# Performance work log

Measured on AMD Instinct MI355X. Metric: run time of the kernel, lower is better.

## Reference

```python
import jax, jax.numpy as jnp
import numpy as np

N = 50000   # nodes
E = 800000  # edges (avg degree 16)
D = 128     # in_dim == hidden_dim


def setup_inputs() -> dict:
    key = jax.random.key(0)
    ks = jax.random.split(key, 8)
    x = jax.random.normal(ks[0], (N, D), dtype=jnp.float32)
    edge_index = jax.random.randint(ks[1], (2, E), 0, N, dtype=jnp.int32)
    s = 1.0 / np.sqrt(D)  # glorot-ish scale
    W0 = jax.random.normal(ks[2], (D, D), dtype=jnp.float32) * s
    W1 = jax.random.normal(ks[3], (D, D), dtype=jnp.float32) * s
    W2 = jax.random.normal(ks[4], (D, D), dtype=jnp.float32) * s
    b0 = jnp.zeros((D,), dtype=jnp.float32)
    b1 = jnp.zeros((D,), dtype=jnp.float32)
    b2 = jnp.zeros((D,), dtype=jnp.float32)
    return {"x": x, "edge_index": edge_index,
            "W0": W0, "b0": b0, "W1": W1, "b1": b1, "W2": W2, "b2": b2}


def reference(x, edge_index, W0, b0, W1, b1, W2, b2):
    # PyG GCNConv defaults: add self-loops, symmetric D^-1/2 (A+I) D^-1/2 norm,
    # linear transform first, bias added after aggregation.
    src, dst = edge_index[0], edge_index[1]
    loops = jnp.arange(N, dtype=src.dtype)
    src_f = jnp.concatenate([src, loops])  # [E+N]
    dst_f = jnp.concatenate([dst, loops])
    deg = jax.ops.segment_sum(jnp.ones_like(src_f, dtype=x.dtype), dst_f, num_segments=N)
    dinv = jnp.where(deg > 0, jax.lax.rsqrt(deg), 0.0)
    norm = dinv[src_f] * dinv[dst_f]  # [E+N]

    def gcn_layer(h, W, b):
        h = h @ W                                # [N, D]
        msg = h[src_f] * norm[:, None]           # [E+N, D] gather
        agg = jax.ops.segment_sum(msg, dst_f, num_segments=N)  # scatter-add
        return agg + b

    h = jax.nn.relu(gcn_layer(x, W0, b0))  # dropout p=0.0 is a no-op
    h = jax.nn.relu(gcn_layer(h, W1, b1))
    return gcn_layer(h, W2, b2)
```

## Files before the change

kernel.cpp:

```cpp
#include <hip/hip_runtime.h>
#include <hip/hip_fp16.h>

#define NN 50000
#define NPAD 50048
#define NE 800000
#define D 128
#define BPAD 136
#define EGRID 3125
#define NB 196
#define GGRID 782

typedef __attribute__((ext_vector_type(8))) short bf16x8;
typedef __attribute__((ext_vector_type(4))) float f32x4;

__device__ inline unsigned short f2bf(float f) {
    unsigned int b = __float_as_uint(f);
    return (unsigned short)((b + 0x7FFFu + ((b >> 16) & 1u)) >> 16);
}
__device__ inline float bf2f(unsigned short u) {
    return __uint_as_float(((unsigned int)u) << 16);
}


__global__ void k_degree_convW(const int* __restrict__ dst, int* __restrict__ cnt,
                               int* __restrict__ rank, int* __restrict__ counter,
                               const float* __restrict__ W0, const float* __restrict__ W1,
                               const float* __restrict__ W2,
                               unsigned short* __restrict__ Wh, unsigned short* __restrict__ Wl) {
    int bid = blockIdx.x;
    int t = threadIdx.x;
    if (bid == 0 && t == 0) counter[0] = 0;
    if (bid < EGRID) {
        int e = bid * 256 + t;
        if (e < NE) {
            int d = dst[e];
            int r = atomicAdd(&cnt[d], 1);
            __builtin_nontemporal_store(r, &rank[e]);
        }
    } else {
        int i = (bid - EGRID) * 256 + t;
        if (i >= 3 * D * D) return;
        int m = i / (D * D), r = i - m * (D * D);
        const float* W = (m == 0) ? W0 : ((m == 1) ? W1 : W2);
        int k = r >> 7, c = r & 127;
        float v = W[r];
        unsigned short h = f2bf(v);
        unsigned short l = f2bf(v - bf2f(h));
        Wh[(size_t)m * D * D + c * D + k] = h;
        Wl[(size_t)m * D * D + c * D + k] = l;
    }
}

__global__ void k_scan_block(const int* __restrict__ cnt, int* __restrict__ excl,
                             int* __restrict__ bsum, int* __restrict__ boff,
                             int* __restrict__ counter) {
    __shared__ int sm[256];
    __shared__ int lastflag;
    int t = threadIdx.x;
    int idx = blockIdx.x * 256 + t;
    int v = (idx < NN) ? cnt[idx] : 0;
    sm[t] = v;
    __syncthreads();
    for (int o = 1; o < 256; o <<= 1) {
        int u = (t >= o) ? sm[t - o] : 0;
        __syncthreads();
        sm[t] += u;
        __syncthreads();
    }
    if (idx < NN) excl[idx] = sm[t] - v;
    if (t == 255) bsum[blockIdx.x] = sm[255];
    __threadfence();
    if (t == 0) {
        int ticket = atomicAdd(counter, 1);
        lastflag = (ticket == NB - 1);
    }
    __syncthreads();
    if (!lastflag) return;
    __threadfence();
    int v2 = (t < NB) ? bsum[t] : 0;
    sm[t] = v2;
    __syncthreads();
    for (int o = 1; o < 256; o <<= 1) {
        int u = (t >= o) ? sm[t - o] : 0;
        __syncthreads();
        sm[t] += u;
        __syncthreads();
    }
    if (t < NB) boff[t] = sm[t] - v2;
}


__device__ inline void gemm_store(f32x4 acc[2][4], const int* __restrict__ cnt,
                                  __half* __restrict__ C, int R0, int C0, int lr, int lg) {
    #pragma unroll
    for (int fr = 0; fr < 2; fr++) {
        int rb = R0 + fr * 16 + lg * 4;
        #pragma unroll
        for (int j = 0; j < 4; j++) {
            int r = rb + j;
            if (r < NN) {
                float s = rsqrtf((float)(cnt[r] + 1));
                #pragma unroll
                for (int fc = 0; fc < 4; fc++)
                    C[(size_t)r * D + C0 + fc * 16 + lr] =
                        __float2half_rn(acc[fr][fc][j] * s);
            }
        }
    }
}


__global__ __launch_bounds__(256, 2) void k_fill_gemm_x(
        const int* __restrict__ src, const int* __restrict__ dst,
        const int* __restrict__ excl, const int* __restrict__ boff,
        const int* __restrict__ rank, int* __restrict__ col,
        const float* __restrict__ X,
        const unsigned short* __restrict__ BhT, const unsigned short* __restrict__ BlT,
        const int* __restrict__ cnt, __half* __restrict__ C) {
    __shared__ short Bs_h[D * BPAD];
    int t = threadIdx.x;
    if (blockIdx.x >= GGRID) {
        int e = (blockIdx.x - GGRID) * 256 + t;
        if (e < NE) {
            int d = dst[e];
            int pos = excl[d] + boff[d >> 8] + rank[e];
            __builtin_nontemporal_store(src[e], &col[pos]);
        }
        return;
    }
    {
        int c = t >> 1;
        int k0 = (t & 1) * 64;
        const unsigned short* gh = BhT + c * D + k0;
        short* dh = Bs_h + c * BPAD + k0;
        #pragma unroll
        for (int i = 0; i < 8; i++)
            *(int4*)(dh + i * 8) = *(const int4*)(gh + i * 8);
    }
    __syncthreads();

    int w = t >> 6, ln = t & 63;
    int wr = w >> 1, wc = w & 1;
    int R0 = blockIdx.x * 64 + wr * 32;
    int C0 = wc * 64;
    int lr = ln & 15, lg = ln >> 4;

    f32x4 acc[2][4];
    #pragma unroll
    for (int a = 0; a < 2; a++)
        #pragma unroll
        for (int b = 0; b < 4; b++)
            acc[a][b] = (f32x4){0.f, 0.f, 0.f, 0.f};

    const float* Ab = X + (size_t)(R0 + lr) * D + lg * 8;

    #pragma unroll
    for (int ks = 0; ks < 4; ks++) {
        int ko = ks * 32;
        bf16x8 fa_h[2], fa_l[2], fb_h[4], fb_l[4];
        #pragma unroll
        for (int fr = 0; fr < 2; fr++) {
            float4 p0 = *(const float4*)(Ab + fr * 16 * D + ko);
            float4 p1 = *(const float4*)(Ab + fr * 16 * D + ko + 4);
            float vv[8] = {p0.x, p0.y, p0.z, p0.w, p1.x, p1.y, p1.z, p1.w};
            #pragma unroll
            for (int j = 0; j < 8; j++) {
                unsigned short h = f2bf(vv[j]);
                fa_h[fr][j] = (short)h;
                fa_l[fr][j] = (short)f2bf(vv[j] - bf2f(h));
            }
        }
        #pragma unroll
        for (int fc = 0; fc < 4; fc++) {
            int ccol = C0 + fc * 16 + lr;
            fb_h[fc] = *(const bf16x8*)(Bs_h + ccol * BPAD + ko + lg * 8);
            fb_l[fc] = *(const bf16x8*)(BlT + (size_t)ccol * D + ko + lg * 8);
        }
        #pragma unroll
        for (int fr = 0; fr < 2; fr++) {
            #pragma unroll
            for (int fc = 0; fc < 4; fc++) {
                acc[fr][fc] = __builtin_amdgcn_mfma_f32_16x16x32_bf16(
                    fa_h[fr], fb_h[fc], acc[fr][fc], 0, 0, 0);
                acc[fr][fc] = __builtin_amdgcn_mfma_f32_16x16x32_bf16(
                    fa_l[fr], fb_h[fc], acc[fr][fc], 0, 0, 0);
                acc[fr][fc] = __builtin_amdgcn_mfma_f32_16x16x32_bf16(
                    fa_h[fr], fb_l[fc], acc[fr][fc], 0, 0, 0);
            }
        }
    }
    gemm_store(acc, cnt, C, R0, C0, lr, lg);
}


__global__ __launch_bounds__(256, 4) void k_gemm_mfma_h(
        const __half* __restrict__ H,
        const unsigned short* __restrict__ BhT, const unsigned short* __restrict__ BlT,
        const int* __restrict__ cnt, __half* __restrict__ C) {
    __shared__ short Bs_h[D * BPAD];
    int t = threadIdx.x;
    {
        int c = t >> 1;
        int k0 = (t & 1) * 64;
        const unsigned short* gh = BhT + c * D + k0;
        short* dh = Bs_h + c * BPAD + k0;
        #pragma unroll
        for (int i = 0; i < 8; i++)
            *(int4*)(dh + i * 8) = *(const int4*)(gh + i * 8);
    }
    __syncthreads();

    int w = t >> 6, ln = t & 63;
    int wr = w >> 1, wc = w & 1;
    int R0 = blockIdx.x * 64 + wr * 32;
    int C0 = wc * 64;
    int lr = ln & 15, lg = ln >> 4;

    f32x4 acc[2][4];
    #pragma unroll
    for (int a = 0; a < 2; a++)
        #pragma unroll
        for (int b = 0; b < 4; b++)
            acc[a][b] = (f32x4){0.f, 0.f, 0.f, 0.f};

    const __half* Ab = H + (size_t)(R0 + lr) * D + lg * 8;

    #pragma unroll
    for (int ks = 0; ks < 4; ks++) {
        int ko = ks * 32;
        bf16x8 fa_h[2], fa_l[2], fb_h[4], fb_l[4];
        #pragma unroll
        for (int fr = 0; fr < 2; fr++) {
            float4 p = *(const float4*)(Ab + fr * 16 * D + ko);
            const __half2* hp = (const __half2*)&p;
            #pragma unroll
            for (int q = 0; q < 4; q++) {
                float2 fv = __half22float2(hp[q]);
                unsigned short h0 = f2bf(fv.x), h1 = f2bf(fv.y);
                fa_h[fr][q * 2]     = (short)h0;
                fa_h[fr][q * 2 + 1] = (short)h1;
                fa_l[fr][q * 2]     = (short)f2bf(fv.x - bf2f(h0));
                fa_l[fr][q * 2 + 1] = (short)f2bf(fv.y - bf2f(h1));
            }
        }
        #pragma unroll
        for (int fc = 0; fc < 4; fc++) {
            int ccol = C0 + fc * 16 + lr;
            fb_h[fc] = *(const bf16x8*)(Bs_h + ccol * BPAD + ko + lg * 8);
            fb_l[fc] = *(const bf16x8*)(BlT + (size_t)ccol * D + ko + lg * 8);
        }
        #pragma unroll
        for (int fr = 0; fr < 2; fr++) {
            #pragma unroll
            for (int fc = 0; fc < 4; fc++) {
                acc[fr][fc] = __builtin_amdgcn_mfma_f32_16x16x32_bf16(
                    fa_h[fr], fb_h[fc], acc[fr][fc], 0, 0, 0);
                acc[fr][fc] = __builtin_amdgcn_mfma_f32_16x16x32_bf16(
                    fa_l[fr], fb_h[fc], acc[fr][fc], 0, 0, 0);
                acc[fr][fc] = __builtin_amdgcn_mfma_f32_16x16x32_bf16(
                    fa_h[fr], fb_l[fc], acc[fr][fc], 0, 0, 0);
            }
        }
    }
    gemm_store(acc, cnt, C, R0, C0, lr, lg);
}


__device__ inline void agg_accum(const float4& rv, float a[8]) {
    const __half2* hp = (const __half2*)&rv;
    #pragma unroll
    for (int q = 0; q < 4; q++) {
        float2 fv = __half22float2(hp[q]);
        a[q * 2] += fv.x;
        a[q * 2 + 1] += fv.y;
    }
}

__device__ inline void agg_core(const __half* __restrict__ T,
                                const int* __restrict__ excl,
                                const int* __restrict__ boff,
                                const int* __restrict__ col,
                                int i, int f, int lane, float a[8]) {
    int gb = lane & 48;
    int sl16 = lane & 15;
    {
        float4 raw = *(const float4*)(T + (size_t)i * D + f);
        const __half2* hp = (const __half2*)&raw;
        #pragma unroll
        for (int q = 0; q < 4; q++) {
            float2 fv = __half22float2(hp[q]);
            a[q * 2] = fv.x;
            a[q * 2 + 1] = fv.y;
        }
    }
    int r0 = excl[i] + boff[i >> 8];
    int r1 = (i == NN - 1) ? NE : (excl[i + 1] + boff[(i + 1) >> 8]);
    for (int e = r0; e < r1; e += 16) {
        int idx = e + sl16;
        if (idx > r1 - 1) idx = r1 - 1;
        int cv = col[idx];
        int m = r1 - e;
        m = m > 16 ? 16 : m;
        int ss[16];
        #pragma unroll
        for (int u = 0; u < 16; u++) ss[u] = __shfl(cv, gb + u, 64);
        float4 rv[16];
        #pragma unroll
        for (int u = 0; u < 16; u++)
            rv[u] = *(const float4*)(T + (size_t)ss[u] * D + f);
        #pragma unroll
        for (int u = 0; u < 16; u++)
            if (u < m) agg_accum(rv[u], a);
    }
}

__global__ __launch_bounds__(256) void k_agg_relu(const __half* __restrict__ T,
                                                  const int* __restrict__ excl,
                                                  const int* __restrict__ boff,
                                                  const int* __restrict__ col,
                                                  const int* __restrict__ cnt,
                                                  const float* __restrict__ bias,
                                                  __half* __restrict__ Hout) {
    int i = blockIdx.x * 16 + (threadIdx.x >> 4);
    int lane = threadIdx.x & 63;
    int sl = threadIdx.x & 15;
    int f = sl * 8;
    float di = rsqrtf((float)(cnt[i] + 1));
    float a[8];
    agg_core(T, excl, boff, col, i, f, lane, a);
    float4 bv0 = *(const float4*)(bias + f);
    float4 bv1 = *(const float4*)(bias + f + 4);
    float bb[8] = {bv0.x, bv0.y, bv0.z, bv0.w, bv1.x, bv1.y, bv1.z, bv1.w};
    __half2 o[4];
    #pragma unroll
    for (int q = 0; q < 4; q++) {
        float x0 = fmaxf(a[q * 2] * di + bb[q * 2], 0.f);
        float x1 = fmaxf(a[q * 2 + 1] * di + bb[q * 2 + 1], 0.f);
        o[q] = __floats2half2_rn(x0, x1);
    }
    *(float4*)(Hout + (size_t)i * D + f) = *(float4*)o;
}

__global__ __launch_bounds__(256) void k_agg_out(const __half* __restrict__ T,
                                                 const int* __restrict__ excl,
                                                 const int* __restrict__ boff,
                                                 const int* __restrict__ col,
                                                 const int* __restrict__ cnt,
                                                 const float* __restrict__ bias,
                                                 float* __restrict__ Of) {
    int i = blockIdx.x * 16 + (threadIdx.x >> 4);
    int lane = threadIdx.x & 63;
    int sl = threadIdx.x & 15;
    int f = sl * 8;
    float di = rsqrtf((float)(cnt[i] + 1));
    float a[8];
    agg_core(T, excl, boff, col, i, f, lane, a);
    float4 bv0 = *(const float4*)(bias + f);
    float4 bv1 = *(const float4*)(bias + f + 4);
    float4 o0 = make_float4(a[0] * di + bv0.x, a[1] * di + bv0.y,
                            a[2] * di + bv0.z, a[3] * di + bv0.w);
    float4 o1 = make_float4(a[4] * di + bv1.x, a[5] * di + bv1.y,
                            a[6] * di + bv1.z, a[7] * di + bv1.w);
    *(float4*)(Of + (size_t)i * D + f) = o0;
    *(float4*)(Of + (size_t)i * D + f + 4) = o1;
}


extern "C" void kernel_launch(void* const* d_in, const int* in_sizes, int n_in,
                              void* d_out, int out_size, void* d_ws, size_t ws_size,
                              hipStream_t stream) {
    const float* x  = (const float*)d_in[0];
    const int* edge = (const int*)d_in[1];
    const float* W0 = (const float*)d_in[2];
    const float* b0 = (const float*)d_in[3];
    const float* W1 = (const float*)d_in[4];
    const float* b1 = (const float*)d_in[5];
    const float* W2 = (const float*)d_in[6];
    const float* b2 = (const float*)d_in[7];
    const int* src = edge;
    const int* dst = edge + NE;
    float* out = (float*)d_out;

    char* ws = (char*)d_ws;
    size_t off = 0;
    auto alloc = [&](size_t bytes) {
        void* p = ws + off;
        off += (bytes + 255) & ~(size_t)255;
        return p;
    };
    int*   cnt     = (int*)alloc(NN * 4);
    int*   counter = (int*)alloc(256);
    int*   excl    = (int*)alloc(NN * 4);
    int*   bsum    = (int*)alloc(256 * 4);
    int*   boff    = (int*)alloc(256 * 4);
    int*   rank    = (int*)alloc((size_t)NE * 4);
    int*   col     = (int*)alloc((size_t)NE * 4);
    unsigned short* Wh = (unsigned short*)alloc(3 * D * D * 2);
    unsigned short* Wl = (unsigned short*)alloc(3 * D * D * 2);
    __half* Ta = (__half*)alloc((size_t)NPAD * D * 2);
    __half* Tb = (__half*)alloc((size_t)NPAD * D * 2);
    __half* Hb = (__half*)alloc((size_t)NPAD * D * 2);

    hipMemsetAsync(cnt, 0, NN * 4, stream);

    k_degree_convW<<<EGRID + 192, 256, 0, stream>>>(dst, cnt, rank, counter,
                                                    W0, W1, W2, Wh, Wl);
    k_scan_block<<<NB, 256, 0, stream>>>(cnt, excl, bsum, boff, counter);

    const int agrid = NN / 16;

    k_fill_gemm_x<<<GGRID + EGRID, 256, 0, stream>>>(src, dst, excl, boff, rank, col,
                                                     x, Wh, Wl, cnt, Ta);
    k_agg_relu<<<agrid, 256, 0, stream>>>(Ta, excl, boff, col, cnt, b0, Hb);
    k_gemm_mfma_h<<<GGRID, 256, 0, stream>>>(Hb, Wh + D * D, Wl + D * D, cnt, Tb);
    k_agg_relu<<<agrid, 256, 0, stream>>>(Tb, excl, boff, col, cnt, b1, Hb);
    k_gemm_mfma_h<<<GGRID, 256, 0, stream>>>(Hb, Wh + 2 * D * D, Wl + 2 * D * D, cnt, Ta);
    k_agg_out<<<agrid, 256, 0, stream>>>(Ta, excl, boff, col, cnt, b2, out);
}
```

Baseline: 230.8 us.

## Bucket CSR neighbor lists by source-node slice for gather locality

Degree counting now keys each edge by destination and by which quarter of the node range its source falls in, and the scan runs over the four-way counts. Within each row, neighbors are grouped by source slice. This is meant to improve cache locality of the feature gathers in the aggregation kernels. Degree is now derived from the row offsets instead of a separate count array, which adds an extra offsets load in the GEMM store epilogue.

```diff
diff --git a/kernel.cpp b/kernel.cpp
--- a/kernel.cpp
+++ b/kernel.cpp
@@ -9,6 +9,8 @@
 #define EGRID 3125
 #define NB 196
 #define GGRID 782
+#define SLICE 12500
+#define FLAT4 (4*NN)
 
 typedef __attribute__((ext_vector_type(8))) short bf16x8;
 typedef __attribute__((ext_vector_type(4))) float f32x4;
@@ -22,7 +24,8 @@
 }
 
 
-__global__ void k_degree_convW(const int* __restrict__ dst, int* __restrict__ cnt,
+__global__ void k_degree_convW(const int* __restrict__ src, const int* __restrict__ dst,
+                               int* __restrict__ cnt4,
                                int* __restrict__ rank, int* __restrict__ counter,
                                const float* __restrict__ W0, const float* __restrict__ W1,
                                const float* __restrict__ W2,
@@ -34,7 +37,8 @@
         int e = bid * 256 + t;
         if (e < NE) {
             int d = dst[e];
-            int r = atomicAdd(&cnt[d], 1);
+            int s = src[e] / SLICE;
+            int r = atomicAdd(&cnt4[d * 4 + s], 1);
             __builtin_nontemporal_store(r, &rank[e]);
         }
     } else {
@@ -51,15 +55,17 @@
     }
 }
 
-__global__ void k_scan_block(const int* __restrict__ cnt, int* __restrict__ excl,
-                             int* __restrict__ bsum, int* __restrict__ boff,
-                             int* __restrict__ counter) {
+__global__ void k_scan_block4(const int* __restrict__ cnt4, int* __restrict__ excl4,
+                              int* __restrict__ bsum, int* __restrict__ boff,
+                              int* __restrict__ counter) {
     __shared__ int sm[256];
     __shared__ int lastflag;
     int t = threadIdx.x;
-    int idx = blockIdx.x * 256 + t;
-    int v = (idx < NN) ? cnt[idx] : 0;
-    sm[t] = v;
+    int base = blockIdx.x * 1024 + t * 4;
+    int4 v = make_int4(0, 0, 0, 0);
+    if (base < FLAT4) v = *(const int4*)(cnt4 + base);
+    int s = v.x + v.y + v.z + v.w;
+    sm[t] = s;
     __syncthreads();
     for (int o = 1; o < 256; o <<= 1) {
         int u = (t >= o) ? sm[t - o] : 0;
@@ -67,7 +73,15 @@
         sm[t] += u;
         __syncthreads();
     }
-    if (idx < NN) excl[idx] = sm[t] - v;
+    int te = sm[t] - s;
+    if (base < FLAT4) {
+        int4 w;
+        w.x = te;
+        w.y = te + v.x;
+        w.z = te + v.x + v.y;
+        w.w = te + v.x + v.y + v.z;
+        *(int4*)(excl4 + base) = w;
+    }
     if (t == 255) bsum[blockIdx.x] = sm[255];
     __threadfence();
     if (t == 0) {
@@ -89,8 +103,19 @@
     if (t < NB) boff[t] = sm[t] - v2;
 }
 
-
-__device__ inline void gemm_store(f32x4 acc[2][4], const int* __restrict__ cnt,
+__device__ inline int row_start(const int* __restrict__ excl4,
+                                const int* __restrict__ boff, int i) {
+    return excl4[i * 4] + boff[i >> 8];
+}
+__device__ inline int row_end(const int* __restrict__ excl4,
+                              const int* __restrict__ boff, int i) {
+    return (i == NN - 1) ? NE : (excl4[(i + 1) * 4] + boff[(i + 1) >> 8]);
+}
+
+
+__device__ inline void gemm_store(f32x4 acc[2][4],
+                                  const int* __restrict__ excl4,
+                                  const int* __restrict__ boff,
                                   __half* __restrict__ C, int R0, int C0, int lr, int lg) {
     #pragma unroll
     for (int fr = 0; fr < 2; fr++) {
@@ -99,7 +124,8 @@
         for (int j = 0; j < 4; j++) {
             int r = rb + j;
             if (r < NN) {
-                float s = rsqrtf((float)(cnt[r] + 1));
+                int deg = row_end(excl4, boff, r) - row_start(excl4, boff, r);
+                float s = rsqrtf((float)(deg + 1));
                 #pragma unroll
                 for (int fc = 0; fc < 4; fc++)
                     C[(size_t)r * D + C0 + fc * 16 + lr] =
@@ -112,19 +138,21 @@
 
 __global__ __launch_bounds__(256, 2) void k_fill_gemm_x(
         const int* __restrict__ src, const int* __restrict__ dst,
-        const int* __restrict__ excl, const int* __restrict__ boff,
+        const int* __restrict__ excl4, const int* __restrict__ boff,
         const int* __restrict__ rank, int* __restrict__ col,
         const float* __restrict__ X,
         const unsigned short* __restrict__ BhT, const unsigned short* __restrict__ BlT,
-        const int* __restrict__ cnt, __half* __restrict__ C) {
+        __half* __restrict__ C) {
     __shared__ short Bs_h[D * BPAD];
     int t = threadIdx.x;
     if (blockIdx.x >= GGRID) {
         int e = (blockIdx.x - GGRID) * 256 + t;
         if (e < NE) {
+            int sv = src[e];
             int d = dst[e];
-            int pos = excl[d] + boff[d >> 8] + rank[e];
-            __builtin_nontemporal_store(src[e], &col[pos]);
+            int sl = sv / SLICE;
+            int pos = excl4[d * 4 + sl] + boff[d >> 8] + rank[e];
+            __builtin_nontemporal_store(sv, &col[pos]);
         }
         return;
     }
@@ -189,14 +217,15 @@
             }
         }
     }
-    gemm_store(acc, cnt, C, R0, C0, lr, lg);
+    gemm_store(acc, excl4, boff, C, R0, C0, lr, lg);
 }
 
 
 __global__ __launch_bounds__(256, 4) void k_gemm_mfma_h(
         const __half* __restrict__ H,
         const unsigned short* __restrict__ BhT, const unsigned short* __restrict__ BlT,
-        const int* __restrict__ cnt, __half* __restrict__ C) {
+        const int* __restrict__ excl4, const int* __restrict__ boff,
+        __half* __restrict__ C) {
     __shared__ short Bs_h[D * BPAD];
     int t = threadIdx.x;
     {
@@ -262,7 +291,7 @@
             }
         }
     }
-    gemm_store(acc, cnt, C, R0, C0, lr, lg);
+    gemm_store(acc, excl4, boff, C, R0, C0, lr, lg);
 }
 
 
@@ -277,10 +306,10 @@
 }
 
 __device__ inline void agg_core(const __half* __restrict__ T,
-                                const int* __restrict__ excl,
+                                const int* __restrict__ excl4,
                                 const int* __restrict__ boff,
                                 const int* __restrict__ col,
-                                int i, int f, int lane, float a[8]) {
+                                int i, int f, int lane, float a[8], int* degOut) {
     int gb = lane & 48;
     int sl16 = lane & 15;
     {
@@ -293,8 +322,9 @@
             a[q * 2 + 1] = fv.y;
         }
     }
-    int r0 = excl[i] + boff[i >> 8];
-    int r1 = (i == NN - 1) ? NE : (excl[i + 1] + boff[(i + 1) >> 8]);
+    int r0 = row_start(excl4, boff, i);
+    int r1 = row_end(excl4, boff, i);
+    *degOut = r1 - r0;
     for (int e = r0; e < r1; e += 16) {
         int idx = e + sl16;
         if (idx > r1 - 1) idx = r1 - 1;
@@ -315,19 +345,19 @@
 }
 
 __global__ __launch_bounds__(256) void k_agg_relu(const __half* __restrict__ T,
-                                                  const int* __restrict__ excl,
+                                                  const int* __restrict__ excl4,
                                                   const int* __restrict__ boff,
                                                   const int* __restrict__ col,
-                                                  const int* __restrict__ cnt,
                                                   const float* __restrict__ bias,
                                                   __half* __restrict__ Hout) {
     int i = blockIdx.x * 16 + (threadIdx.x >> 4);
     int lane = threadIdx.x & 63;
     int sl = threadIdx.x & 15;
     int f = sl * 8;
-    float di = rsqrtf((float)(cnt[i] + 1));
     float a[8];
-    agg_core(T, excl, boff, col, i, f, lane, a);
+    int deg;
+    agg_core(T, excl4, boff, col, i, f, lane, a, &deg);
+    float di = rsqrtf((float)(deg + 1));
     float4 bv0 = *(const float4*)(bias + f);
     float4 bv1 = *(const float4*)(bias + f + 4);
     float bb[8] = {bv0.x, bv0.y, bv0.z, bv0.w, bv1.x, bv1.y, bv1.z, bv1.w};
@@ -342,19 +372,19 @@
 }
 
 __global__ __launch_bounds__(256) void k_agg_out(const __half* __restrict__ T,
-                                                 const int* __restrict__ excl,
+                                                 const int* __restrict__ excl4,
                                                  const int* __restrict__ boff,
                                                  const int* __restrict__ col,
-                                                 const int* __restrict__ cnt,
                                                  const float* __restrict__ bias,
                                                  float* __restrict__ Of) {
     int i = blockIdx.x * 16 + (threadIdx.x >> 4);
     int lane = threadIdx.x & 63;
     int sl = threadIdx.x & 15;
     int f = sl * 8;
-    float di = rsqrtf((float)(cnt[i] + 1));
     float a[8];
-    agg_core(T, excl, boff, col, i, f, lane, a);
+    int deg;
+    agg_core(T, excl4, boff, col, i, f, lane, a, &deg);
+    float di = rsqrtf((float)(deg + 1));
     float4 bv0 = *(const float4*)(bias + f);
     float4 bv1 = *(const float4*)(bias + f + 4);
     float4 o0 = make_float4(a[0] * di + bv0.x, a[1] * di + bv0.y,
@@ -388,9 +418,9 @@
         off += (bytes + 255) & ~(size_t)255;
         return p;
     };
-    int*   cnt     = (int*)alloc(NN * 4);
+    int*   cnt4    = (int*)alloc((size_t)FLAT4 * 4);
     int*   counter = (int*)alloc(256);
-    int*   excl    = (int*)alloc(NN * 4);
+    int*   excl4   = (int*)alloc((size_t)FLAT4 * 4);
     int*   bsum    = (int*)alloc(256 * 4);
     int*   boff    = (int*)alloc(256 * 4);
     int*   rank    = (int*)alloc((size_t)NE * 4);
@@ -401,19 +431,20 @@
     __half* Tb = (__half*)alloc((size_t)NPAD * D * 2);
     __half* Hb = (__half*)alloc((size_t)NPAD * D * 2);
 
-    hipMemsetAsync(cnt, 0, NN * 4, stream);
-
-    k_degree_convW<<<EGRID + 192, 256, 0, stream>>>(dst, cnt, rank, counter,
+    hipMemsetAsync(cnt4, 0, (size_t)FLAT4 * 4, stream);
+
+    k_degree_convW<<<EGRID + 192, 256, 0, stream>>>(src, dst, cnt4, rank, counter,
                                                     W0, W1, W2, Wh, Wl);
-    k_scan_block<<<NB, 256, 0, stream>>>(cnt, excl, bsum, boff, counter);
+    k_scan_block4<<<NB, 256, 0, stream>>>(cnt4, excl4, bsum, boff, counter);
 
     const int agrid = NN / 16;
 
-    k_fill_gemm_x<<<GGRID + EGRID, 256, 0, stream>>>(src, dst, excl, boff, rank, col,
-                                                     x, Wh, Wl, cnt, Ta);
-    k_agg_relu<<<agrid, 256, 0, stream>>>(Ta, excl, boff, col, cnt, b0, Hb);
-    k_gemm_mfma_h<<<GGRID, 256, 0, stream>>>(Hb, Wh + D * D, Wl + D * D, cnt, Tb);
-    k_agg_relu<<<agrid, 256, 0, stream>>>(Tb, excl, boff, col, cnt, b1, Hb);
-    k_gemm_mfma_h<<<GGRID, 256, 0, stream>>>(Hb, Wh + 2 * D * D, Wl + 2 * D * D, cnt, Ta);
-    k_agg_out<<<agrid, 256, 0, stream>>>(Ta, excl, boff, col, cnt, b2, out);
-}
+    k_fill_gemm_x<<<GGRID + EGRID, 256, 0, stream>>>(src, dst, excl4, boff, rank, col,
+                                                     x, Wh, Wl, Ta);
+    k_agg_relu<<<agrid, 256, 0, stream>>>(Ta, excl4, boff, col, b0, Hb);
+    k_gemm_mfma_h<<<GGRID, 256, 0, stream>>>(Hb, Wh + D * D, Wl + D * D, excl4, boff, Tb);
+    k_agg_relu<<<agrid, 256, 0, stream>>>(Tb, excl4, boff, col, b1, Hb);
+    k_gemm_mfma_h<<<GGRID, 256, 0, stream>>>(Hb, Wh + 2 * D * D, Wl + 2 * D * D,
+                                             excl4, boff, Ta);
+    k_agg_out<<<agrid, 256, 0, stream>>>(Ta, excl4, boff, col, b2, out);
+}
```

Measured after the change: 231.0 us. No clear change (+0.1%).
